# Kernel optimization log

Measured on AMD Instinct MI355X. Metric: run time of the kernel, lower is better.

## Reference

```python
import jax, jax.numpy as jnp
import numpy as np

B = 131072            # number of supervoxel areas (vmapped)
H, W = 8, 16          # mask_new / mask_old shape
DX, DY = 16, 16       # diameter_x, diameter_y -> mask_combined / image shape
DIM_STRIDE = 0
TV = 2                # translation_val


def _grad(x, axis):
    # numpy-style gradient, unit spacing: central diff interior, one-sided edges
    x = jnp.moveaxis(x, axis, 0)
    g = jnp.concatenate([x[1:2] - x[0:1], (x[2:] - x[:-2]) * 0.5, x[-1:] - x[-2:-1]], axis=0)
    return jnp.moveaxis(g, 0, axis)


def get_diamond(diameter):
    r = diameter // 2
    def line(curr, idx):
        return jax.lax.dynamic_update_slice(curr, jnp.ones(diameter, jnp.float32), (jnp.abs(r - idx),))
    a = jax.vmap(line)(jnp.zeros((diameter, 2 * diameter), jnp.float32), jnp.arange(diameter)).astype(bool)
    b = jnp.flip(a)[:, diameter:]   # flip over both axes, keep right half
    a = a[:, :-diameter]
    return jnp.logical_and(a, b).astype(jnp.float32)


def translate(mask, axis, is_forward, tv, shape):
    lo = tv * (1 - is_forward)
    hi = shape[axis] - tv * is_forward
    m = jnp.take(mask, jnp.arange(lo, hi), axis=axis)
    pad = [[0, 0], [0, 0]]
    pad[axis][1 - is_forward] = tv
    return jnp.pad(m, pad)


def features(image, mask):
    mi = image * mask
    s = jnp.sum(mask)
    mean = jnp.sum(mi) / s
    var = jnp.sum(((mi - mean) * mask) ** 2) / s
    return jnp.stack([mean, var])


def single(image, mn, mo, diamond):
    # consistency loss
    p = jnp.pad(mo, ((1, 1), (1, 1)))
    g = _grad(p, DIM_STRIDE) ** 2
    g = g[1:-1, 1:-1]
    consistency = jnp.mean(jnp.maximum(mn - (g * 5.0 + mo * 5.0), 0.0))
    # intertwine 'f h w -> (h f) w'
    mc = jnp.stack([mn, mo], axis=1).reshape(DX, DY)
    rounding = jnp.mean(-((mc - (1.0 - mc)) ** 2))
    feats = jnp.stack([
        features(image, translate(mc, 0, 0, TV, (DX, DY))),
        features(image, translate(mc, 0, 1, TV, (DX, DY))),
        features(image, translate(mc, 1, 0, TV, (DX, DY))),
        features(image, translate(mc, 1, 1, TV, (DX, DY)))])
    fvar = jnp.mean(jnp.var(feats, axis=0))
    gi = _grad(image, DIM_STRIDE)
    gm = _grad(mc, DIM_STRIDE)
    edge = jnp.mean(0.5 * (gi - gm) ** 2 * gi)   # optax.l2_loss scaled by image gradient
    avg_cov = jnp.mean(0.5 * (mc - diamond) ** 2)
    mi = mc * image
    out_image = mc * (jnp.sum(mi) / jnp.sum(mc))
    return mc, out_image, consistency, rounding, fvar, edge, avg_cov


def setup_inputs() -> dict:
    key = jax.random.key(0)
    k1, k2, k3 = jax.random.split(key, 3)
    return {
        "resized_image": jax.random.normal(k1, (B, DX, DY), jnp.float32),
        "mask_new": jax.random.uniform(k2, (B, H, W), jnp.float32),
        "mask_old": jax.random.uniform(k3, (B, H, W), jnp.float32),
    }


def reference(resized_image, mask_new, mask_old):
    diamond = jnp.pad(get_diamond(DX - 1), ((0, 1), (0, 1)))  # (DX, DY)
    return jax.vmap(lambda im, mn, mo: single(im, mn, mo, diamond))(resized_image, mask_new, mask_old)
```

## Files before the change

### kernel.cpp

```cpp
#include <hip/hip_runtime.h>

typedef float vf2 __attribute__((ext_vector_type(2)));

template<int CTRL>
__device__ __forceinline__ float dppf(float v) {
    return __int_as_float(__builtin_amdgcn_update_dpp(
        0, __float_as_int(v), CTRL, 0xF, 0xF, true));
}

__device__ __forceinline__ float bfly8(float v) {
    v += dppf<0xB1>(v);
    v += dppf<0x4E>(v);
    v += dppf<0x141>(v);
    return v;
}

__global__ __launch_bounds__(256, 3) void apply_area_kernel(
    const float* __restrict__ img_g,
    const float* __restrict__ mn_g,
    const float* __restrict__ mo_g,
    float* __restrict__ out,
    int B)
{
    const int lane = threadIdx.x & 63;
    const int w    = threadIdx.x >> 6;
    const int q    = lane >> 3;
    const int l    = lane & 7;
    const int b    = blockIdx.x * 32 + w * 8 + q;
    if (b >= B) return;

    const vf2* im2 = reinterpret_cast<const vf2*>(img_g) + (size_t)b * 128 + l;
    const vf2* mn2 = reinterpret_cast<const vf2*>(mn_g)  + (size_t)b * 64  + l;
    const vf2* mo2 = reinterpret_cast<const vf2*>(mo_g)  + (size_t)b * 64  + l;

    float imx[16], imy[16], mcx[16], mcy[16];
#pragma unroll
    for (int r = 0; r < 16; ++r) { vf2 v = im2[r * 8]; imx[r] = v.x; imy[r] = v.y; }
#pragma unroll
    for (int i = 0; i < 8; ++i) {
        vf2 a = mn2[i * 8]; mcx[2*i]   = a.x; mcy[2*i]   = a.y;
        vf2 o = mo2[i * 8]; mcx[2*i+1] = o.x; mcy[2*i+1] = o.y;
    }
    asm volatile("" ::: "memory");

    float c_acc = 0.f;
#pragma unroll
    for (int i = 0; i < 8; ++i) {
        float mx_m = (i > 0) ? mcx[2*i-1] : 0.f, my_m = (i > 0) ? mcy[2*i-1] : 0.f;
        float mx_p = (i < 7) ? mcx[2*i+3] : 0.f, my_p = (i < 7) ? mcy[2*i+3] : 0.f;
        float gx = 0.5f * (mx_p - mx_m), gy = 0.5f * (my_p - my_m);
        c_acc += fmaxf(mcx[2*i] - 5.f * (gx*gx + mcx[2*i+1]), 0.f);
        c_acc += fmaxf(mcy[2*i] - 5.f * (gy*gy + mcy[2*i+1]), 0.f);
    }

    float e_acc = 0.f, r_acc = 0.f, a_acc = 0.f, smi = 0.f, S1 = 0.f, S2 = 0.f;
    const int c0 = 2 * l, c1 = 2 * l + 1;
#pragma unroll
    for (int r = 0; r < 16; ++r) {
        int abr = (r > 7) ? r - 7 : 7 - r;
        bool drow = (r < 15);
#define COMP(imA, mcA, cc) { \
        float gi = (r == 0)  ? imA[1] - imA[0] \
                 : (r == 15) ? imA[15] - imA[14] \
                 : 0.5f * (imA[r + 1] - imA[r - 1]); \
        float gm = (r == 0)  ? mcA[1] - mcA[0] \
                 : (r == 15) ? mcA[15] - mcA[14] \
                 : 0.5f * (mcA[r + 1] - mcA[r - 1]); \
        float d = gi - gm; e_acc += 0.5f * d * d * gi; \
        float tw = 2.f * mcA[r] - 1.f; r_acc += tw * tw; \
        float dia = (drow && (cc) >= abr && (cc) <= 14 - abr) ? 1.f : 0.f; \
        float dd = mcA[r] - dia; a_acc += 0.5f * dd * dd; \
        S1 += mcA[r]; S2 += mcA[r] * mcA[r]; smi += mcA[r] * imA[r]; }
        COMP(imx, mcx, c0)
        COMP(imy, mcy, c1)
#undef COMP
    }

    const float mz7 = (l == 7) ? 0.f : 1.f;
    const float mz0 = (l == 0) ? 0.f : 1.f;
    float B0=0,D0=0,E0=0, B1=0,D1=0,E1=0, B2=0,D2=0,E2=0, B3=0,D3=0,E3=0;
#pragma unroll
    for (int r = 0; r < 16; ++r) {
        float t0x = (r < 14) ? mcx[r+2] : 0.f, t0y = (r < 14) ? mcy[r+2] : 0.f;
        float t1x = (r >= 2) ? mcx[r-2] : 0.f, t1y = (r >= 2) ? mcy[r-2] : 0.f;
        float t2x = dppf<0x101>(mcx[r]) * mz7, t2y = dppf<0x101>(mcy[r]) * mz7;
        float t3x = dppf<0x111>(mcx[r]) * mz0, t3y = dppf<0x111>(mcy[r]) * mz0;
#define ACC2(tx, ty, Bx, Dx, Ex) { \
        float mix_ = (tx) * imx[r], miy_ = (ty) * imy[r]; \
        Bx += mix_ + miy_; \
        Dx += (tx)*(tx)*mix_ + (ty)*(ty)*miy_; \
        float ax_ = (tx)*mix_, ay_ = (ty)*miy_; \
        Ex += ax_*ax_ + ay_*ay_; }
        ACC2(t0x, t0y, B0, D0, E0)
        ACC2(t1x, t1y, B1, D1, E1)
        ACC2(t2x, t2y, B2, D2, E2)
        ACC2(t3x, t3y, B3, D3, E3)
#undef ACC2
    }
    float A0 = S1 - (mcx[0] + mcy[0] + mcx[1] + mcy[1]);
    float C0 = S2 - (mcx[0]*mcx[0] + mcy[0]*mcy[0] + mcx[1]*mcx[1] + mcy[1]*mcy[1]);
    float A1 = S1 - (mcx[14] + mcy[14] + mcx[15] + mcy[15]);
    float C1 = S2 - (mcx[14]*mcx[14] + mcy[14]*mcy[14] + mcx[15]*mcx[15] + mcy[15]*mcy[15]);
    float A2 = dppf<0x101>(S1) * mz7, C2 = dppf<0x101>(S2) * mz7;
    float A3 = dppf<0x111>(S1) * mz0, C3 = dppf<0x111>(S2) * mz0;

    c_acc = bfly8(c_acc); r_acc = bfly8(r_acc);
    e_acc = bfly8(e_acc); a_acc = bfly8(a_acc);
    float smc = bfly8(S1); smi = bfly8(smi);
    A0 = bfly8(A0); A1 = bfly8(A1); A2 = bfly8(A2); A3 = bfly8(A3);
    B0 = bfly8(B0); B1 = bfly8(B1); B2 = bfly8(B2); B3 = bfly8(B3);
    C0 = bfly8(C0); C1 = bfly8(C1); C2 = bfly8(C2); C3 = bfly8(C3);
    D0 = bfly8(D0); D1 = bfly8(D1); D2 = bfly8(D2); D3 = bfly8(D3);
    E0 = bfly8(E0); E1 = bfly8(E1); E2 = bfly8(E2); E3 = bfly8(E3);

    const float scale = smi / smc;
    vf2* mco = reinterpret_cast<vf2*>(out) + (size_t)b * 128 + l;
    vf2* oio = reinterpret_cast<vf2*>(out) + (size_t)B * 128 + (size_t)b * 128 + l;
#pragma unroll
    for (int r = 0; r < 16; ++r) {
        vf2 mv; mv.x = mcx[r]; mv.y = mcy[r];
        vf2 ov; ov.x = mcx[r] * scale; ov.y = mcy[r] * scale;
        __builtin_nontemporal_store(mv, mco + r * 8);
        __builtin_nontemporal_store(ov, oio + r * 8);
    }

    if (l == 0) {
        float m0 = B0 / A0, m1 = B1 / A1, m2 = B2 / A2, m3 = B3 / A3;
        float v0 = (E0 - 2.f * m0 * D0 + m0 * m0 * C0) / A0;
        float v1 = (E1 - 2.f * m1 * D1 + m1 * m1 * C1) / A1;
        float v2 = (E2 - 2.f * m2 * D2 + m2 * m2 * C2) / A2;
        float v3 = (E3 - 2.f * m3 * D3 + m3 * m3 * C3) / A3;

        float fm = 0.25f * (m0 + m1 + m2 + m3);
        float dm0 = m0 - fm, dm1 = m1 - fm, dm2 = m2 - fm, dm3 = m3 - fm;
        float vm = 0.25f * (dm0*dm0 + dm1*dm1 + dm2*dm2 + dm3*dm3);
        float fv = 0.25f * (v0 + v1 + v2 + v3);
        float dv0 = v0 - fv, dv1 = v1 - fv, dv2 = v2 - fv, dv3 = v3 - fv;
        float vv = 0.25f * (dv0*dv0 + dv1*dv1 + dv2*dv2 + dv3*dv3);

        float* s = out + (size_t)B * 512;
        __builtin_nontemporal_store(c_acc * (1.f / 128.f), s + b);
        __builtin_nontemporal_store(-r_acc * (1.f / 256.f), s + (size_t)B + b);
        __builtin_nontemporal_store(0.5f * (vm + vv), s + 2*(size_t)B + b);
        __builtin_nontemporal_store(e_acc * (1.f / 256.f), s + 3*(size_t)B + b);
        __builtin_nontemporal_store(a_acc * (1.f / 256.f), s + 4*(size_t)B + b);
    }
}

extern "C" void kernel_launch(void* const* d_in, const int* in_sizes, int n_in,
                              void* d_out, int out_size, void* d_ws, size_t ws_size,
                              hipStream_t stream) {
    const float* img = (const float*)d_in[0];
    const float* mn  = (const float*)d_in[1];
    const float* mo  = (const float*)d_in[2];
    float* out = (float*)d_out;
    const int B = in_sizes[0] / 256;
    const int blocks = (B + 31) / 32;
    apply_area_kernel<<<blocks, 256, 0, stream>>>(img, mn, mo, out, B);
}
```

Measured before the change: 101.6 us.

## Process four items per wave with double-buffered register tiles

Each wave group now handles four supervoxel areas strided across the grid. It loads the next tile into a second register buffer while computing and storing the current one, so global load latency overlaps with compute. The grid shrinks fourfold and launch bounds drop to two blocks per CU to make room for the doubled register footprint. The cost is lower occupancy and higher register pressure, with a risk of spills.

```diff
diff --git a/kernel.cpp b/kernel.cpp
--- a/kernel.cpp
+++ b/kernel.cpp
@@ -15,33 +15,29 @@
     return v;
 }
 
-__global__ __launch_bounds__(256, 3) void apply_area_kernel(
-    const float* __restrict__ img_g,
-    const float* __restrict__ mn_g,
-    const float* __restrict__ mo_g,
-    float* __restrict__ out,
-    int B)
-{
-    const int lane = threadIdx.x & 63;
-    const int w    = threadIdx.x >> 6;
-    const int q    = lane >> 3;
-    const int l    = lane & 7;
-    const int b    = blockIdx.x * 32 + w * 8 + q;
-    if (b >= B) return;
+struct Tile {
+    float imx[16], imy[16], mcx[16], mcy[16];
+};
 
+__device__ __forceinline__ void load_tile(Tile& t,
+        const float* __restrict__ img_g, const float* __restrict__ mn_g,
+        const float* __restrict__ mo_g, int b, int l) {
     const vf2* im2 = reinterpret_cast<const vf2*>(img_g) + (size_t)b * 128 + l;
     const vf2* mn2 = reinterpret_cast<const vf2*>(mn_g)  + (size_t)b * 64  + l;
     const vf2* mo2 = reinterpret_cast<const vf2*>(mo_g)  + (size_t)b * 64  + l;
-
-    float imx[16], imy[16], mcx[16], mcy[16];
 #pragma unroll
-    for (int r = 0; r < 16; ++r) { vf2 v = im2[r * 8]; imx[r] = v.x; imy[r] = v.y; }
+    for (int r = 0; r < 16; ++r) { vf2 v = im2[r * 8]; t.imx[r] = v.x; t.imy[r] = v.y; }
 #pragma unroll
     for (int i = 0; i < 8; ++i) {
-        vf2 a = mn2[i * 8]; mcx[2*i]   = a.x; mcy[2*i]   = a.y;
-        vf2 o = mo2[i * 8]; mcx[2*i+1] = o.x; mcy[2*i+1] = o.y;
+        vf2 a = mn2[i * 8]; t.mcx[2*i]   = a.x; t.mcy[2*i]   = a.y;
+        vf2 o = mo2[i * 8]; t.mcx[2*i+1] = o.x; t.mcy[2*i+1] = o.y;
     }
-    asm volatile("" ::: "memory");
+}
+
+__device__ __forceinline__ void compute_store(const Tile& t, int b, int B,
+        float* __restrict__ out, int l) {
+    const float (&imx)[16] = t.imx; const float (&imy)[16] = t.imy;
+    const float (&mcx)[16] = t.mcx; const float (&mcy)[16] = t.mcy;
 
     float c_acc = 0.f;
 #pragma unroll
@@ -130,7 +126,6 @@
         float v1 = (E1 - 2.f * m1 * D1 + m1 * m1 * C1) / A1;
         float v2 = (E2 - 2.f * m2 * D2 + m2 * m2 * C2) / A2;
         float v3 = (E3 - 2.f * m3 * D3 + m3 * m3 * C3) / A3;
-
         float fm = 0.25f * (m0 + m1 + m2 + m3);
         float dm0 = m0 - fm, dm1 = m1 - fm, dm2 = m2 - fm, dm3 = m3 - fm;
         float vm = 0.25f * (dm0*dm0 + dm1*dm1 + dm2*dm2 + dm3*dm3);
@@ -147,6 +142,37 @@
     }
 }
 
+__global__ __launch_bounds__(256, 2) void apply_area_kernel(
+    const float* __restrict__ img_g,
+    const float* __restrict__ mn_g,
+    const float* __restrict__ mo_g,
+    float* __restrict__ out,
+    int B, int stride)
+{
+    const int lane = threadIdx.x & 63;
+    const int w    = threadIdx.x >> 6;
+    const int q    = lane >> 3;
+    const int l    = lane & 7;
+    const int b0   = blockIdx.x * 32 + w * 8 + q;
+    const int b1 = b0 + stride, b2 = b1 + stride, b3 = b2 + stride;
+
+    Tile A, Bt;
+    if (b0 < B) load_tile(A, img_g, mn_g, mo_g, b0, l);
+    if (b1 < B) load_tile(Bt, img_g, mn_g, mo_g, b1, l);
+    asm volatile("" ::: "memory");
+    if (b0 < B) compute_store(A, b0, B, out, l);
+
+    if (b2 < B) load_tile(A, img_g, mn_g, mo_g, b2, l);
+    asm volatile("" ::: "memory");
+    if (b1 < B) compute_store(Bt, b1, B, out, l);
+
+    if (b3 < B) load_tile(Bt, img_g, mn_g, mo_g, b3, l);
+    asm volatile("" ::: "memory");
+    if (b2 < B) compute_store(A, b2, B, out, l);
+
+    if (b3 < B) compute_store(Bt, b3, B, out, l);
+}
+
 extern "C" void kernel_launch(void* const* d_in, const int* in_sizes, int n_in,
                               void* d_out, int out_size, void* d_ws, size_t ws_size,
                               hipStream_t stream) {
@@ -155,6 +181,7 @@
     const float* mo  = (const float*)d_in[2];
     float* out = (float*)d_out;
     const int B = in_sizes[0] / 256;
-    const int blocks = (B + 31) / 32;
-    apply_area_kernel<<<blocks, 256, 0, stream>>>(img, mn, mo, out, B);
+    const int blocks = (B + 127) / 128;
+    const int stride = blocks * 32;
+    apply_area_kernel<<<blocks, 256, 0, stream>>>(img, mn, mo, out, B, stride);
 }
```

Result: slower. 110.1 us (+8.4%).
